# Kernel optimization log

Measured on AMD Instinct MI355X. Metric: run time of the kernel, lower is better.

The kernel has to match this reference:

```python
import jax, jax.numpy as jnp
import numpy as np

N_ITEMS = 7000
N_USERS = 30000
N_NODES = N_ITEMS + N_USERS  # 37000
D = 128        # embed_dim == user_embed_dim
E = 400000     # num edges
R = 10         # n_relation (num ratings)
NB = 8         # num_bases
B = 512        # batch of conversations
L = 100        # max context items per sample


def setup_inputs() -> dict:
    key = jax.random.key(0)
    ks = jax.random.split(key, 16)
    # edges: item (source) -> user (target), disjoint id ranges as in load_data
    src = jax.random.randint(ks[0], (E,), 0, N_ITEMS)
    dst = jax.random.randint(ks[1], (E,), N_ITEMS, N_NODES)
    edge_index = jnp.stack([src, dst]).astype(jnp.int64)
    edge_type = jax.random.randint(ks[2], (E,), 0, R).astype(jnp.int64)

    def make_ctx(k1, k2):
        c = jax.random.randint(k1, (B, L), 0, N_ITEMS)
        drop = jax.random.uniform(k2, (B, L)) < 0.3  # -1 padding as in batch lists
        return jnp.where(drop, -1, c).astype(jnp.int64)

    ctx_init = make_ctx(ks[3], ks[4])
    ctx_resp = make_ctx(ks[5], ks[6])

    s = 0.02
    basis = jax.random.normal(ks[7], (NB, N_NODES, D), jnp.float32) * s
    comp = jax.random.normal(ks[8], (R, NB), jnp.float32) * s
    root = jax.random.normal(ks[9], (N_NODES, D), jnp.float32) * s
    bias = jnp.zeros((D,), jnp.float32)
    attn_a = jax.random.normal(ks[10], (D, D), jnp.float32) * s
    attn_b = jax.random.normal(ks[11], (D,), jnp.float32) * s
    fc1_w = jax.random.normal(ks[12], (D, D), jnp.float32) * s
    fc1_b = jnp.zeros((D,), jnp.float32)
    fc2_w = jax.random.normal(ks[13], (D, D), jnp.float32) * s
    fc2_b = jnp.zeros((D,), jnp.float32)
    efc1_w = jax.random.normal(ks[14], (2 * D, D), jnp.float32) * s
    efc1_b = jnp.zeros((D,), jnp.float32)
    efc2_w = jax.random.normal(ks[15], (D, D), jnp.float32) * s
    efc2_b = jnp.zeros((D,), jnp.float32)
    return dict(edge_index=edge_index, edge_type=edge_type, ctx_init=ctx_init,
                ctx_resp=ctx_resp, basis=basis, comp=comp, root=root, bias=bias,
                attn_a=attn_a, attn_b=attn_b, fc1_w=fc1_w, fc1_b=fc1_b,
                fc2_w=fc2_w, fc2_b=fc2_b, efc1_w=efc1_w, efc1_b=efc1_b,
                efc2_w=efc2_w, efc2_b=efc2_b)


def _rgcn(basis, comp, root, bias, edge_index, edge_type):
    # RGCNConv with x=None: per-edge message W_{r_e}[src_e], mean-aggregated
    # per (target, relation), summed over relations, plus root lookup + bias.
    src, dst = edge_index[0], edge_index[1]
    nb, n, d = basis.shape
    r = comp.shape[0]
    cpe = comp[edge_type]  # [E, NB]
    msg = jnp.zeros((src.shape[0], d), basis.dtype)
    for b in range(nb):  # small fixed basis count; avoids [E,NB,D] gather
        msg = msg + cpe[:, b:b + 1] * basis[b][src]
    seg = dst * r + edge_type  # per-(node, relation) segment for mean aggr
    sums = jax.ops.segment_sum(msg, seg, num_segments=n * r).reshape(n, r, d)
    cnt = jax.ops.segment_sum(jnp.ones_like(edge_type, basis.dtype), seg,
                              num_segments=n * r).reshape(n, r, 1)
    return root + bias + (sums / jnp.maximum(cnt, 1.0)).sum(axis=1)  # [N, D]


def _item_user_means(node_emb, edge_index):
    # mean over users connected to each item (edge_idx[1][edge_idx[0]==item])
    src, dst = edge_index[0], edge_index[1]
    isum = jax.ops.segment_sum(node_emb[dst], src, num_segments=N_ITEMS)
    icnt = jax.ops.segment_sum(jnp.ones_like(src, node_emb.dtype), src,
                               num_segments=N_ITEMS)
    item_mean = isum / jnp.maximum(icnt, 1.0)[:, None]  # [N_ITEMS, D]
    return item_mean, icnt > 0


def _attn_pool(ctx, item_mean, item_has_users, attn_a, attn_b):
    # SelfAttentionBatch over each sample's item reps (padding/-1 & degree-0
    # items masked out; all-empty samples -> zeros, as in original).
    valid = ctx >= 0
    idx = jnp.clip(ctx, 0, N_ITEMS - 1)
    h = item_mean[idx]                       # [B, L, D]
    valid = valid & item_has_users[idx]
    e = jnp.einsum('bld,d->bl', jnp.tanh(jnp.einsum('bld,de->ble', h, attn_a)),
                   attn_b)
    attn = jax.nn.softmax(jnp.where(valid, e, -1e9), axis=-1)
    attn = jnp.where(valid, attn, 0.0)
    return jnp.einsum('bl,bld->bd', attn, h)  # [B, D]


def _project(x, w1, b1, w2, b2):
    # fc1 -> relu -> fc2 -> relu (as in _project_user_interaction_*)
    return jax.nn.relu(jax.nn.relu(x @ w1 + b1) @ w2 + b2)


def reference(edge_index, edge_type, ctx_init, ctx_resp, basis, comp, root,
              bias, attn_a, attn_b, fc1_w, fc1_b, fc2_w, fc2_b, efc1_w,
              efc1_b, efc2_w, efc2_b):
    node_emb = _rgcn(basis, comp, root, bias, edge_index, edge_type)
    item_mean, item_has = _item_user_means(node_emb, edge_index)
    p_init = _project(_attn_pool(ctx_init, item_mean, item_has, attn_a, attn_b),
                      fc1_w, fc1_b, fc2_w, fc2_b)
    p_resp = _project(_attn_pool(ctx_resp, item_mean, item_has, attn_a, attn_b),
                      fc1_w, fc1_b, fc2_w, fc2_b)
    both = jnp.concatenate([p_init, p_resp], axis=1)  # [B, 2D]
    profile = _project(both, efc1_w, efc1_b, efc2_w, efc2_b)  # [B, D]
    return profile, p_init, p_resp
```

## Files before the change

### kernel.cpp

```cpp
#include <hip/hip_runtime.h>
#include <math.h>

typedef unsigned int uint;

#define N_ITEMS 7000
#define N_NODES 37000
#define N_USERS 30000
#define DIM     128
#define HD      64
#define NREL    10
#define NBASES  8
#define BATCH   512
#define CTXL    100
#define E_MAX   400000

#define UCAP    64
#define ICAP    128

#define OFF_CNT    0
#define OFF_ICNT   (OFF_CNT + N_USERS * NREL)
#define OFF_UCNT   (OFF_ICNT + N_ITEMS)
#define ZERO_ELEMS (OFF_UCNT + N_USERS)
#define OFF_ICSR   ZERO_ELEMS
#define OFF_UCSR   (OFF_ICSR + N_ITEMS * ICAP)
#define OFF_WC     (OFF_UCSR + N_USERS * UCAP)
#define OFF_ACC    (OFF_WC + NREL * N_ITEMS * HD)
#define OFF_MEAN   (OFF_ACC + N_USERS * HD)
#define OFF_SCORE  (OFF_MEAN + N_ITEMS * HD)

__device__ __forceinline__ float2 bf2f(uint p) {
  float2 r;
  r.x = __uint_as_float(p << 16);
  r.y = __uint_as_float(p & 0xffff0000u);
  return r;
}
__device__ __forceinline__ uint f2bf(float x, float y) {
  uint a = __float_as_uint(x), b = __float_as_uint(y);
  a += 0x7fffu + ((a >> 16) & 1u);
  b += 0x7fffu + ((b >> 16) & 1u);
  return (a >> 16) | (b & 0xffff0000u);
}

__device__ __forceinline__ float wave_sum(float v) {
#pragma unroll
  for (int o = 1; o < 64; o <<= 1) v += __shfl_xor(v, o, 64);
  return v;
}
__device__ __forceinline__ float wave_max(float v) {
#pragma unroll
  for (int o = 1; o < 64; o <<= 1) v = fmaxf(v, __shfl_xor(v, o, 64));
  return v;
}

#define COMBINE_BLOCKS (N_ITEMS / 4)
__global__ __launch_bounds__(256) void k_initfill(const float* __restrict__ basis,
                                                  const float* __restrict__ comp,
                                                  uint* __restrict__ Wc,
                                                  const int* __restrict__ ei,
                                                  const int* __restrict__ et, int E,
                                                  int* __restrict__ cnt,
                                                  int* __restrict__ icnt,
                                                  int* __restrict__ ucnt,
                                                  int* __restrict__ icsr,
                                                  int* __restrict__ ucsr) {
  int tid = threadIdx.x;
  if (blockIdx.x < COMBINE_BLOCKS) {
    int i = blockIdx.x * 4 + (tid >> 6);
    int lane = tid & 63;
    float2 bb[NBASES];
#pragma unroll
    for (int b = 0; b < NBASES; ++b)
      bb[b] = ((const float2*)basis)[((size_t)b * N_NODES + i) * HD + lane];
#pragma unroll
    for (int r = 0; r < NREL; ++r) {
      float sx = 0.f, sy = 0.f;
#pragma unroll
      for (int b = 0; b < NBASES; ++b) {
        float c = comp[r * NBASES + b];
        sx = fmaf(c, bb[b].x, sx);
        sy = fmaf(c, bb[b].y, sy);
      }
      Wc[((size_t)i * NREL + r) * HD + lane] = f2bf(sx, sy);
    }
  } else {
    int e = (blockIdx.x - COMBINE_BLOCKS) * 256 + tid;
    if (e < E) {
      int s  = ei[e];
      int u0 = ei[E + e] - N_ITEMS;
      int t  = et[e];
      atomicAdd(&cnt[u0 * NREL + t], 1);
      int si = atomicAdd(&icnt[s], 1);
      if (si < ICAP) icsr[s * ICAP + si] = u0;
      int su = atomicAdd(&ucnt[u0], 1);
      if (su < UCAP) ucsr[u0 * UCAP + su] = s | (t << 16);
    }
  }
}

__global__ __launch_bounds__(256, 4) void k_useragg(const int* __restrict__ ucnt,
                                                    const int* __restrict__ ucsr,
                                                    const int* __restrict__ cnt,
                                                    const uint* __restrict__ Wc,
                                                    const float* __restrict__ root,
                                                    uint* __restrict__ acc) {
  int tid = threadIdx.x;
  int wid = tid >> 6, lane = tid & 63;
  int uA = blockIdx.x * 8 + wid * 2;
  int uB = uA + 1;
  int degA = ucnt[uA]; if (degA > UCAP) degA = UCAP;
  int degB = ucnt[uB]; if (degB > UCAP) degB = UCAP;
  float wlA = 0.f, wlB = 0.f;
  if (lane < NREL) {
    int cA = cnt[uA * NREL + lane];
    int cB = cnt[uB * NREL + lane];
    wlA = (cA > 0) ? 1.0f / (float)cA : 0.0f;
    wlB = (cB > 0) ? 1.0f / (float)cB : 0.0f;
  }
  int plA = ucsr[uA * UCAP + lane];
  int plB = ucsr[uB * UCAP + lane];

  float2 avA[4], avB[4];
#pragma unroll
  for (int k = 0; k < 4; ++k) {
    avA[k].x = 0.f; avA[k].y = 0.f;
    avB[k].x = 0.f; avB[k].y = 0.f;
  }
  int mmax = (degA > degB) ? degA : degB;
#pragma unroll 1
  for (int kk = 0; kk < mmax; kk += 16) {
    uint qA[16], qB[16];
#pragma unroll
    for (int k = 0; k < 16; ++k) {
      int idx = kk + k;
      int p = (idx < degA) ? __shfl(plA, idx & 63) : 0;
      qA[k] = Wc[((size_t)(p & 0xffff) * NREL + (p >> 16)) * HD + lane];
    }
#pragma unroll
    for (int k = 0; k < 16; ++k) {
      int idx = kk + k;
      int p = (idx < degB) ? __shfl(plB, idx & 63) : 0;
      qB[k] = Wc[((size_t)(p & 0xffff) * NREL + (p >> 16)) * HD + lane];
    }
#pragma unroll
    for (int k = 0; k < 16; ++k) {
      int idx = kk + k;
      int p = __shfl(plA, idx & 63);
      float w = (idx < degA) ? __shfl(wlA, p >> 16) : 0.f;
      float2 f = bf2f(qA[k]);
      avA[k & 3].x = fmaf(w, f.x, avA[k & 3].x);
      avA[k & 3].y = fmaf(w, f.y, avA[k & 3].y);
    }
#pragma unroll
    for (int k = 0; k < 16; ++k) {
      int idx = kk + k;
      int p = __shfl(plB, idx & 63);
      float w = (idx < degB) ? __shfl(wlB, p >> 16) : 0.f;
      float2 f = bf2f(qB[k]);
      avB[k & 3].x = fmaf(w, f.x, avB[k & 3].x);
      avB[k & 3].y = fmaf(w, f.y, avB[k & 3].y);
    }
  }
  float2 rtA = ((const float2*)root)[(size_t)(N_ITEMS + uA) * HD + lane];
  float2 rtB = ((const float2*)root)[(size_t)(N_ITEMS + uB) * HD + lane];
  rtA.x += (avA[0].x + avA[1].x) + (avA[2].x + avA[3].x);
  rtA.y += (avA[0].y + avA[1].y) + (avA[2].y + avA[3].y);
  rtB.x += (avB[0].x + avB[1].x) + (avB[2].x + avB[3].x);
  rtB.y += (avB[0].y + avB[1].y) + (avB[2].y + avB[3].y);
  acc[(size_t)uA * HD + lane] = f2bf(rtA.x, rtA.y);
  acc[(size_t)uB * HD + lane] = f2bf(rtB.x, rtB.y);
}

__global__ __launch_bounds__(256, 4) void k_itemagg(const int* __restrict__ icnt,
                                                    const int* __restrict__ icsr,
                                                    const uint* __restrict__ acc,
                                                    const float* __restrict__ bias,
                                                    const float* __restrict__ attn_a,
                                                    const float* __restrict__ attn_b,
                                                    uint* __restrict__ mean,
                                                    float* __restrict__ score) {
  int tid = threadIdx.x;
  int wid = tid >> 6, lane = tid & 63;
  int iA = blockIdx.x * 8 + wid * 2;
  int iB = iA + 1;
  int degA = icnt[iA], degB = icnt[iB];
  int dcA = (degA > ICAP) ? ICAP : degA;
  int dcB = (degB > ICAP) ? ICAP : degB;
  int plA0 = icsr[iA * ICAP + lane];
  int plA1 = icsr[iA * ICAP + 64 + lane];
  int plB0 = icsr[iB * ICAP + lane];
  int plB1 = icsr[iB * ICAP + 64 + lane];

  float2 avA[4], avB[4];
#pragma unroll
  for (int k = 0; k < 4; ++k) {
    avA[k].x = 0.f; avA[k].y = 0.f;
    avB[k].x = 0.f; avB[k].y = 0.f;
  }
  int mmax = (dcA > dcB) ? dcA : dcB;
#pragma unroll 1
  for (int kk = 0; kk < mmax; kk += 16) {
    int plAc = (kk < 64) ? plA0 : plA1;
    int plBc = (kk < 64) ? plB0 : plB1;
    uint qA[16], qB[16];
#pragma unroll
    for (int k = 0; k < 16; ++k) {
      int idx = kk + k;
      int u0 = (idx < dcA) ? __shfl(plAc, idx & 63) : 0;
      qA[k] = acc[(size_t)u0 * HD + lane];
    }
#pragma unroll
    for (int k = 0; k < 16; ++k) {
      int idx = kk + k;
      int u0 = (idx < dcB) ? __shfl(plBc, idx & 63) : 0;
      qB[k] = acc[(size_t)u0 * HD + lane];
    }
#pragma unroll
    for (int k = 0; k < 16; ++k) {
      int idx = kk + k;
      float w = (idx < dcA) ? 1.0f : 0.0f;
      float2 f = bf2f(qA[k]);
      avA[k & 3].x = fmaf(w, f.x, avA[k & 3].x);
      avA[k & 3].y = fmaf(w, f.y, avA[k & 3].y);
    }
#pragma unroll
    for (int k = 0; k < 16; ++k) {
      int idx = kk + k;
      float w = (idx < dcB) ? 1.0f : 0.0f;
      float2 f = bf2f(qB[k]);
      avB[k & 3].x = fmaf(w, f.x, avB[k & 3].x);
      avB[k & 3].y = fmaf(w, f.y, avB[k & 3].y);
    }
  }
  float sxA = (avA[0].x + avA[1].x) + (avA[2].x + avA[3].x);
  float syA = (avA[0].y + avA[1].y) + (avA[2].y + avA[3].y);
  float sxB = (avB[0].x + avB[1].x) + (avB[2].x + avB[3].x);
  float syB = (avB[0].y + avB[1].y) + (avB[2].y + avB[3].y);
  float2 bv = ((const float2*)bias)[lane];
  float2 mvA = {0.f, 0.f}, mvB = {0.f, 0.f};
  if (degA > 0) {
    float inv = 1.0f / (float)degA;
    mvA.x = sxA * inv + bv.x;
    mvA.y = syA * inv + bv.y;
  }
  if (degB > 0) {
    float inv = 1.0f / (float)degB;
    mvB.x = sxB * inv + bv.x;
    mvB.y = syB * inv + bv.y;
  }
  mean[(size_t)iA * HD + lane] = f2bf(mvA.x, mvA.y);
  mean[(size_t)iB * HD + lane] = f2bf(mvB.x, mvB.y);

  float z0A = 0.f, z1A = 0.f, z0B = 0.f, z1B = 0.f;
#pragma unroll 8
  for (int k2 = 0; k2 < HD; ++k2) {
    float2 w0 = ((const float2*)attn_a)[(size_t)(2 * k2) * HD + lane];
    float2 w1 = ((const float2*)attn_a)[(size_t)(2 * k2 + 1) * HD + lane];
    float hxA = __shfl(mvA.x, k2), hyA = __shfl(mvA.y, k2);
    float hxB = __shfl(mvB.x, k2), hyB = __shfl(mvB.y, k2);
    z0A = fmaf(hxA, w0.x, z0A); z1A = fmaf(hxA, w0.y, z1A);
    z0A = fmaf(hyA, w1.x, z0A); z1A = fmaf(hyA, w1.y, z1A);
    z0B = fmaf(hxB, w0.x, z0B); z1B = fmaf(hxB, w0.y, z1B);
    z0B = fmaf(hyB, w1.x, z0B); z1B = fmaf(hyB, w1.y, z1B);
  }
  float2 ab = ((const float2*)attn_b)[lane];
  float vA = wave_sum(tanhf(z0A) * ab.x + tanhf(z1A) * ab.y);
  float vB = wave_sum(tanhf(z0B) * ab.x + tanhf(z1B) * ab.y);
  if (lane == 0) {
    score[iA] = (degA > 0) ? vA : -1e9f;
    score[iB] = (degB > 0) ? vB : -1e9f;
  }
}

__global__ __launch_bounds__(128) void k_batch2(const int* __restrict__ ctx0,
                                                const int* __restrict__ ctx1,
                                                const uint* __restrict__ mean,
                                                const float* __restrict__ score,
                                                const float* __restrict__ fc1_w,
                                                const float* __restrict__ fc1_b,
                                                const float* __restrict__ fc2_w,
                                                const float* __restrict__ fc2_b,
                                                const float* __restrict__ efc1_w,
                                                const float* __restrict__ efc1_b,
                                                const float* __restrict__ efc2_w,
                                                const float* __restrict__ efc2_b,
                                                float* __restrict__ out) {
  __shared__ float2 shp[2][HD];
  int b = blockIdx.x;
  int wv = threadIdx.x >> 6;
  int lane = threadIdx.x & 63;
  float2* out2 = (float2*)out;

  const int* cx = (wv ? ctx1 : ctx0) + (size_t)b * CTXL;
  int id0 = cx[lane];
  float e0 = (id0 >= 0) ? score[id0] : -1e9f;
  int id1 = -1;
  float e1 = -3.0e38f;
  if (lane < CTXL - 64) {
    id1 = cx[64 + lane];
    e1 = (id1 >= 0) ? score[id1] : -1e9f;
  }
  float mx = wave_max(fmaxf(e0, e1));
  float x0 = expf(e0 - mx);
  float x1 = (lane < CTXL - 64) ? expf(e1 - mx) : 0.f;
  float inv = 1.0f / wave_sum(x0 + x1);
  float w0 = (id0 >= 0) ? x0 * inv : 0.f;
  float w1 = (id1 >= 0) ? x1 * inv : 0.f;
  int i0 = (id0 >= 0) ? id0 : 0;
  int i1 = (id1 >= 0) ? id1 : 0;

  float2 av[4];
#pragma unroll
  for (int k = 0; k < 4; ++k) { av[k].x = 0.f; av[k].y = 0.f; }
  for (int j = 0; j < 64; j += 4) {
#pragma unroll
    for (int k = 0; k < 4; ++k) {
      int ii = __shfl(i0, j + k);
      float ww = __shfl(w0, j + k);
      float2 f = bf2f(mean[(size_t)ii * HD + lane]);
      av[k].x = fmaf(ww, f.x, av[k].x);
      av[k].y = fmaf(ww, f.y, av[k].y);
    }
  }
  for (int j = 0; j < CTXL - 64; j += 4) {
#pragma unroll
    for (int k = 0; k < 4; ++k) {
      int ii = __shfl(i1, j + k);
      float ww = __shfl(w1, j + k);
      float2 f = bf2f(mean[(size_t)ii * HD + lane]);
      av[k].x = fmaf(ww, f.x, av[k].x);
      av[k].y = fmaf(ww, f.y, av[k].y);
    }
  }
  float2 pool;
  pool.x = (av[0].x + av[1].x) + (av[2].x + av[3].x);
  pool.y = (av[0].y + av[1].y) + (av[2].y + av[3].y);

  float2 z = ((const float2*)fc1_b)[lane];
#pragma unroll 8
  for (int k2 = 0; k2 < HD; ++k2) {
    float hx = __shfl(pool.x, k2);
    float hy = __shfl(pool.y, k2);
    float2 wa = ((const float2*)fc1_w)[(size_t)(2 * k2) * HD + lane];
    float2 wb = ((const float2*)fc1_w)[(size_t)(2 * k2 + 1) * HD + lane];
    z.x = fmaf(hx, wa.x, z.x); z.y = fmaf(hx, wa.y, z.y);
    z.x = fmaf(hy, wb.x, z.x); z.y = fmaf(hy, wb.y, z.y);
  }
  z.x = fmaxf(z.x, 0.f);
  z.y = fmaxf(z.y, 0.f);

  float2 z2 = ((const float2*)fc2_b)[lane];
#pragma unroll 8
  for (int k2 = 0; k2 < HD; ++k2) {
    float hx = __shfl(z.x, k2);
    float hy = __shfl(z.y, k2);
    float2 wa = ((const float2*)fc2_w)[(size_t)(2 * k2) * HD + lane];
    float2 wb = ((const float2*)fc2_w)[(size_t)(2 * k2 + 1) * HD + lane];
    z2.x = fmaf(hx, wa.x, z2.x); z2.y = fmaf(hx, wa.y, z2.y);
    z2.x = fmaf(hy, wb.x, z2.x); z2.y = fmaf(hy, wb.y, z2.y);
  }
  z2.x = fmaxf(z2.x, 0.f);
  z2.y = fmaxf(z2.y, 0.f);
  out2[((size_t)(1 + wv) * BATCH + b) * HD + lane] = z2;
  shp[wv][lane] = z2;
  __syncthreads();

  if (wv == 0) {
    float2 p0 = shp[0][lane];
    float2 p1 = shp[1][lane];
    float2 zz = ((const float2*)efc1_b)[lane];
#pragma unroll 8
    for (int k2 = 0; k2 < HD; ++k2) {
      float hx = __shfl(p0.x, k2);
      float hy = __shfl(p0.y, k2);
      float2 wa = ((const float2*)efc1_w)[(size_t)(2 * k2) * HD + lane];
      float2 wb = ((const float2*)efc1_w)[(size_t)(2 * k2 + 1) * HD + lane];
      zz.x = fmaf(hx, wa.x, zz.x); zz.y = fmaf(hx, wa.y, zz.y);
      zz.x = fmaf(hy, wb.x, zz.x); zz.y = fmaf(hy, wb.y, zz.y);
    }
#pragma unroll 8
    for (int k2 = 0; k2 < HD; ++k2) {
      float hx = __shfl(p1.x, k2);
      float hy = __shfl(p1.y, k2);
      float2 wa = ((const float2*)efc1_w)[(size_t)(DIM + 2 * k2) * HD + lane];
      float2 wb = ((const float2*)efc1_w)[(size_t)(DIM + 2 * k2 + 1) * HD + lane];
      zz.x = fmaf(hx, wa.x, zz.x); zz.y = fmaf(hx, wa.y, zz.y);
      zz.x = fmaf(hy, wb.x, zz.x); zz.y = fmaf(hy, wb.y, zz.y);
    }
    zz.x = fmaxf(zz.x, 0.f);
    zz.y = fmaxf(zz.y, 0.f);

    float2 zf = ((const float2*)efc2_b)[lane];
#pragma unroll 8
    for (int k2 = 0; k2 < HD; ++k2) {
      float hx = __shfl(zz.x, k2);
      float hy = __shfl(zz.y, k2);
      float2 wa = ((const float2*)efc2_w)[(size_t)(2 * k2) * HD + lane];
      float2 wb = ((const float2*)efc2_w)[(size_t)(2 * k2 + 1) * HD + lane];
      zf.x = fmaf(hx, wa.x, zf.x); zf.y = fmaf(hx, wa.y, zf.y);
      zf.x = fmaf(hy, wb.x, zf.x); zf.y = fmaf(hy, wb.y, zf.y);
    }
    zf.x = fmaxf(zf.x, 0.f);
    zf.y = fmaxf(zf.y, 0.f);
    out2[(size_t)b * HD + lane] = zf;
  }
}

extern "C" void kernel_launch(void* const* d_in, const int* in_sizes, int n_in,
                              void* d_out, int out_size, void* d_ws, size_t ws_size,
                              hipStream_t stream) {
  const int*   ei     = (const int*)d_in[0];
  const int*   et     = (const int*)d_in[1];
  const int*   ctx0   = (const int*)d_in[2];
  const int*   ctx1   = (const int*)d_in[3];
  const float* basis  = (const float*)d_in[4];
  const float* comp   = (const float*)d_in[5];
  const float* root   = (const float*)d_in[6];
  const float* bias   = (const float*)d_in[7];
  const float* attn_a = (const float*)d_in[8];
  const float* attn_b = (const float*)d_in[9];
  const float* fc1_w  = (const float*)d_in[10];
  const float* fc1_b  = (const float*)d_in[11];
  const float* fc2_w  = (const float*)d_in[12];
  const float* fc2_b  = (const float*)d_in[13];
  const float* efc1_w = (const float*)d_in[14];
  const float* efc1_b = (const float*)d_in[15];
  const float* efc2_w = (const float*)d_in[16];
  const float* efc2_b = (const float*)d_in[17];
  float* out = (float*)d_out;

  const int E = in_sizes[1];

  float* ws   = (float*)d_ws;
  int*  cnt   = (int*)(ws + OFF_CNT);
  int*  icnt  = (int*)(ws + OFF_ICNT);
  int*  ucnt  = (int*)(ws + OFF_UCNT);
  int*  icsr  = (int*)(ws + OFF_ICSR);
  int*  ucsr  = (int*)(ws + OFF_UCSR);
  uint* Wc    = (uint*)(ws + OFF_WC);
  uint* acc   = (uint*)(ws + OFF_ACC);
  uint* mean  = (uint*)(ws + OFF_MEAN);
  float* score = ws + OFF_SCORE;

  hipMemsetAsync(d_ws, 0, (size_t)ZERO_ELEMS * sizeof(float), stream);

  int countBlocks = (E + 255) / 256;
  k_initfill<<<COMBINE_BLOCKS + countBlocks, 256, 0, stream>>>(
      basis, comp, Wc, ei, et, E, cnt, icnt, ucnt, icsr, ucsr);
  k_useragg<<<N_USERS / 8, 256, 0, stream>>>(ucnt, ucsr, cnt, Wc, root, acc);
  k_itemagg<<<N_ITEMS / 8, 256, 0, stream>>>(icnt, icsr, acc, bias, attn_a,
                                             attn_b, mean, score);
  k_batch2<<<BATCH, 128, 0, stream>>>(ctx0, ctx1, mean, score, fc1_w, fc1_b,
                                      fc2_w, fc2_b, efc1_w, efc1_b, efc2_w,
                                      efc2_b, out);
}
```

Before: 387.4 us.

## Fuse all stages into one persistent cooperative kernel with grid syncs

Replaces the memset and four separate kernel launches with a single cooperative persistent kernel. Work is distributed with grid-stride loops, and stages are separated by grid.sync plus threadfence. The aim is to remove launch gaps and the separate memset. In exchange, the grid is capped at occupancy-limited block counts, which can reduce parallelism for the gather-heavy stages, and each grid barrier has its own cost.

Result: slower. 1.007 ms (+160.0%).

```diff
diff --git a/kernel.cpp b/kernel.cpp
--- a/kernel.cpp
+++ b/kernel.cpp
@@ -1,5 +1,8 @@
 #include <hip/hip_runtime.h>
+#include <hip/hip_cooperative_groups.h>
 #include <math.h>
+
+namespace cg = cooperative_groups;
 
 typedef unsigned int uint;
 
@@ -52,404 +55,415 @@
   return v;
 }
 
-#define COMBINE_BLOCKS (N_ITEMS / 4)
-__global__ __launch_bounds__(256) void k_initfill(const float* __restrict__ basis,
-                                                  const float* __restrict__ comp,
-                                                  uint* __restrict__ Wc,
-                                                  const int* __restrict__ ei,
-                                                  const int* __restrict__ et, int E,
-                                                  int* __restrict__ cnt,
-                                                  int* __restrict__ icnt,
-                                                  int* __restrict__ ucnt,
-                                                  int* __restrict__ icsr,
-                                                  int* __restrict__ ucsr) {
-  int tid = threadIdx.x;
-  if (blockIdx.x < COMBINE_BLOCKS) {
-    int i = blockIdx.x * 4 + (tid >> 6);
-    int lane = tid & 63;
+struct KParams {
+  const int*   ei;
+  const int*   et;
+  const int*   ctx0;
+  const int*   ctx1;
+  const float* basis;
+  const float* comp;
+  const float* root;
+  const float* bias;
+  const float* attn_a;
+  const float* attn_b;
+  const float* fc1_w;
+  const float* fc1_b;
+  const float* fc2_w;
+  const float* fc2_b;
+  const float* efc1_w;
+  const float* efc1_b;
+  const float* efc2_w;
+  const float* efc2_b;
+  float*       out;
+  float*       ws;
+  int          E;
+};
+
+__global__ __launch_bounds__(256, 4) void k_all(KParams p) {
+  int*  cnt   = (int*)(p.ws + OFF_CNT);
+  int*  icnt  = (int*)(p.ws + OFF_ICNT);
+  int*  ucnt  = (int*)(p.ws + OFF_UCNT);
+  int*  icsr  = (int*)(p.ws + OFF_ICSR);
+  int*  ucsr  = (int*)(p.ws + OFF_UCSR);
+  uint* Wc    = (uint*)(p.ws + OFF_WC);
+  uint* acc   = (uint*)(p.ws + OFF_ACC);
+  uint* mean  = (uint*)(p.ws + OFF_MEAN);
+  float* score = p.ws + OFF_SCORE;
+
+  const int tid  = threadIdx.x;
+  const int lane = tid & 63;
+  const int wid  = tid >> 6;
+  const int gsize = gridDim.x * 256;
+  const int gtid  = blockIdx.x * 256 + tid;
+  const int W  = gridDim.x * 4;
+  const int gw = blockIdx.x * 4 + wid;
+
+  __shared__ float2 shp[2][2][HD];
+
+  cg::grid_group grid = cg::this_grid();
+
+  {
+    int* wsz = (int*)p.ws;
+    for (int i = gtid; i < ZERO_ELEMS; i += gsize) wsz[i] = 0;
+  }
+  __threadfence();
+  grid.sync();
+
+  for (int i = gw; i < N_ITEMS; i += W) {
     float2 bb[NBASES];
 #pragma unroll
     for (int b = 0; b < NBASES; ++b)
-      bb[b] = ((const float2*)basis)[((size_t)b * N_NODES + i) * HD + lane];
+      bb[b] = ((const float2*)p.basis)[((size_t)b * N_NODES + i) * HD + lane];
 #pragma unroll
     for (int r = 0; r < NREL; ++r) {
       float sx = 0.f, sy = 0.f;
 #pragma unroll
       for (int b = 0; b < NBASES; ++b) {
-        float c = comp[r * NBASES + b];
+        float c = p.comp[r * NBASES + b];
         sx = fmaf(c, bb[b].x, sx);
         sy = fmaf(c, bb[b].y, sy);
       }
       Wc[((size_t)i * NREL + r) * HD + lane] = f2bf(sx, sy);
     }
-  } else {
-    int e = (blockIdx.x - COMBINE_BLOCKS) * 256 + tid;
-    if (e < E) {
-      int s  = ei[e];
-      int u0 = ei[E + e] - N_ITEMS;
-      int t  = et[e];
-      atomicAdd(&cnt[u0 * NREL + t], 1);
-      int si = atomicAdd(&icnt[s], 1);
-      if (si < ICAP) icsr[s * ICAP + si] = u0;
-      int su = atomicAdd(&ucnt[u0], 1);
-      if (su < UCAP) ucsr[u0 * UCAP + su] = s | (t << 16);
-    }
-  }
-}
-
-__global__ __launch_bounds__(256, 4) void k_useragg(const int* __restrict__ ucnt,
-                                                    const int* __restrict__ ucsr,
-                                                    const int* __restrict__ cnt,
-                                                    const uint* __restrict__ Wc,
-                                                    const float* __restrict__ root,
-                                                    uint* __restrict__ acc) {
-  int tid = threadIdx.x;
-  int wid = tid >> 6, lane = tid & 63;
-  int uA = blockIdx.x * 8 + wid * 2;
-  int uB = uA + 1;
-  int degA = ucnt[uA]; if (degA > UCAP) degA = UCAP;
-  int degB = ucnt[uB]; if (degB > UCAP) degB = UCAP;
-  float wlA = 0.f, wlB = 0.f;
-  if (lane < NREL) {
-    int cA = cnt[uA * NREL + lane];
-    int cB = cnt[uB * NREL + lane];
-    wlA = (cA > 0) ? 1.0f / (float)cA : 0.0f;
-    wlB = (cB > 0) ? 1.0f / (float)cB : 0.0f;
-  }
-  int plA = ucsr[uA * UCAP + lane];
-  int plB = ucsr[uB * UCAP + lane];
-
-  float2 avA[4], avB[4];
-#pragma unroll
-  for (int k = 0; k < 4; ++k) {
-    avA[k].x = 0.f; avA[k].y = 0.f;
-    avB[k].x = 0.f; avB[k].y = 0.f;
-  }
-  int mmax = (degA > degB) ? degA : degB;
+  }
+  for (int e = gtid; e < p.E; e += gsize) {
+    int s  = p.ei[e];
+    int u0 = p.ei[p.E + e] - N_ITEMS;
+    int t  = p.et[e];
+    atomicAdd(&cnt[u0 * NREL + t], 1);
+    int si = atomicAdd(&icnt[s], 1);
+    if (si < ICAP) icsr[s * ICAP + si] = u0;
+    int su = atomicAdd(&ucnt[u0], 1);
+    if (su < UCAP) ucsr[u0 * UCAP + su] = s | (t << 16);
+  }
+  __threadfence();
+  grid.sync();
+
+  for (int u = gw * 2; u < N_USERS; u += W * 2) {
+    int uA = u, uB = u + 1;
+    int degA = ucnt[uA]; if (degA > UCAP) degA = UCAP;
+    int degB = ucnt[uB]; if (degB > UCAP) degB = UCAP;
+    float wlA = 0.f, wlB = 0.f;
+    if (lane < NREL) {
+      int cA = cnt[uA * NREL + lane];
+      int cB = cnt[uB * NREL + lane];
+      wlA = (cA > 0) ? 1.0f / (float)cA : 0.0f;
+      wlB = (cB > 0) ? 1.0f / (float)cB : 0.0f;
+    }
+    int plA = ucsr[uA * UCAP + lane];
+    int plB = ucsr[uB * UCAP + lane];
+
+    float2 avA[4], avB[4];
+#pragma unroll
+    for (int k = 0; k < 4; ++k) {
+      avA[k].x = 0.f; avA[k].y = 0.f;
+      avB[k].x = 0.f; avB[k].y = 0.f;
+    }
+    int mmax = (degA > degB) ? degA : degB;
 #pragma unroll 1
-  for (int kk = 0; kk < mmax; kk += 16) {
-    uint qA[16], qB[16];
-#pragma unroll
-    for (int k = 0; k < 16; ++k) {
-      int idx = kk + k;
-      int p = (idx < degA) ? __shfl(plA, idx & 63) : 0;
-      qA[k] = Wc[((size_t)(p & 0xffff) * NREL + (p >> 16)) * HD + lane];
-    }
-#pragma unroll
-    for (int k = 0; k < 16; ++k) {
-      int idx = kk + k;
-      int p = (idx < degB) ? __shfl(plB, idx & 63) : 0;
-      qB[k] = Wc[((size_t)(p & 0xffff) * NREL + (p >> 16)) * HD + lane];
-    }
-#pragma unroll
-    for (int k = 0; k < 16; ++k) {
-      int idx = kk + k;
-      int p = __shfl(plA, idx & 63);
-      float w = (idx < degA) ? __shfl(wlA, p >> 16) : 0.f;
-      float2 f = bf2f(qA[k]);
-      avA[k & 3].x = fmaf(w, f.x, avA[k & 3].x);
-      avA[k & 3].y = fmaf(w, f.y, avA[k & 3].y);
-    }
-#pragma unroll
-    for (int k = 0; k < 16; ++k) {
-      int idx = kk + k;
-      int p = __shfl(plB, idx & 63);
-      float w = (idx < degB) ? __shfl(wlB, p >> 16) : 0.f;
-      float2 f = bf2f(qB[k]);
-      avB[k & 3].x = fmaf(w, f.x, avB[k & 3].x);
-      avB[k & 3].y = fmaf(w, f.y, avB[k & 3].y);
-    }
-  }
-  float2 rtA = ((const float2*)root)[(size_t)(N_ITEMS + uA) * HD + lane];
-  float2 rtB = ((const float2*)root)[(size_t)(N_ITEMS + uB) * HD + lane];
-  rtA.x += (avA[0].x + avA[1].x) + (avA[2].x + avA[3].x);
-  rtA.y += (avA[0].y + avA[1].y) + (avA[2].y + avA[3].y);
-  rtB.x += (avB[0].x + avB[1].x) + (avB[2].x + avB[3].x);
-  rtB.y += (avB[0].y + avB[1].y) + (avB[2].y + avB[3].y);
-  acc[(size_t)uA * HD + lane] = f2bf(rtA.x, rtA.y);
-  acc[(size_t)uB * HD + lane] = f2bf(rtB.x, rtB.y);
-}
-
-__global__ __launch_bounds__(256, 4) void k_itemagg(const int* __restrict__ icnt,
-                                                    const int* __restrict__ icsr,
-                                                    const uint* __restrict__ acc,
-                                                    const float* __restrict__ bias,
-                                                    const float* __restrict__ attn_a,
-                                                    const float* __restrict__ attn_b,
-                                                    uint* __restrict__ mean,
-                                                    float* __restrict__ score) {
-  int tid = threadIdx.x;
-  int wid = tid >> 6, lane = tid & 63;
-  int iA = blockIdx.x * 8 + wid * 2;
-  int iB = iA + 1;
-  int degA = icnt[iA], degB = icnt[iB];
-  int dcA = (degA > ICAP) ? ICAP : degA;
-  int dcB = (degB > ICAP) ? ICAP : degB;
-  int plA0 = icsr[iA * ICAP + lane];
-  int plA1 = icsr[iA * ICAP + 64 + lane];
-  int plB0 = icsr[iB * ICAP + lane];
-  int plB1 = icsr[iB * ICAP + 64 + lane];
-
-  float2 avA[4], avB[4];
-#pragma unroll
-  for (int k = 0; k < 4; ++k) {
-    avA[k].x = 0.f; avA[k].y = 0.f;
-    avB[k].x = 0.f; avB[k].y = 0.f;
-  }
-  int mmax = (dcA > dcB) ? dcA : dcB;
+    for (int kk = 0; kk < mmax; kk += 16) {
+      uint qA[16], qB[16];
+#pragma unroll
+      for (int k = 0; k < 16; ++k) {
+        int idx = kk + k;
+        int pp = (idx < degA) ? __shfl(plA, idx & 63) : 0;
+        qA[k] = Wc[((size_t)(pp & 0xffff) * NREL + (pp >> 16)) * HD + lane];
+      }
+#pragma unroll
+      for (int k = 0; k < 16; ++k) {
+        int idx = kk + k;
+        int pp = (idx < degB) ? __shfl(plB, idx & 63) : 0;
+        qB[k] = Wc[((size_t)(pp & 0xffff) * NREL + (pp >> 16)) * HD + lane];
+      }
+#pragma unroll
+      for (int k = 0; k < 16; ++k) {
+        int idx = kk + k;
+        int pp = __shfl(plA, idx & 63);
+        float w = (idx < degA) ? __shfl(wlA, pp >> 16) : 0.f;
+        float2 f = bf2f(qA[k]);
+        avA[k & 3].x = fmaf(w, f.x, avA[k & 3].x);
+        avA[k & 3].y = fmaf(w, f.y, avA[k & 3].y);
+      }
+#pragma unroll
+      for (int k = 0; k < 16; ++k) {
+        int idx = kk + k;
+        int pp = __shfl(plB, idx & 63);
+        float w = (idx < degB) ? __shfl(wlB, pp >> 16) : 0.f;
+        float2 f = bf2f(qB[k]);
+        avB[k & 3].x = fmaf(w, f.x, avB[k & 3].x);
+        avB[k & 3].y = fmaf(w, f.y, avB[k & 3].y);
+      }
+    }
+    float2 rtA = ((const float2*)p.root)[(size_t)(N_ITEMS + uA) * HD + lane];
+    float2 rtB = ((const float2*)p.root)[(size_t)(N_ITEMS + uB) * HD + lane];
+    rtA.x += (avA[0].x + avA[1].x) + (avA[2].x + avA[3].x);
+    rtA.y += (avA[0].y + avA[1].y) + (avA[2].y + avA[3].y);
+    rtB.x += (avB[0].x + avB[1].x) + (avB[2].x + avB[3].x);
+    rtB.y += (avB[0].y + avB[1].y) + (avB[2].y + avB[3].y);
+    acc[(size_t)uA * HD + lane] = f2bf(rtA.x, rtA.y);
+    acc[(size_t)uB * HD + lane] = f2bf(rtB.x, rtB.y);
+  }
+  __threadfence();
+  grid.sync();
+
+  for (int i = gw * 2; i < N_ITEMS; i += W * 2) {
+    int iA = i, iB = i + 1;
+    int degA = icnt[iA], degB = icnt[iB];
+    int dcA = (degA > ICAP) ? ICAP : degA;
+    int dcB = (degB > ICAP) ? ICAP : degB;
+    int plA0 = icsr[iA * ICAP + lane];
+    int plA1 = icsr[iA * ICAP + 64 + lane];
+    int plB0 = icsr[iB * ICAP + lane];
+    int plB1 = icsr[iB * ICAP + 64 + lane];
+
+    float2 avA[4], avB[4];
+#pragma unroll
+    for (int k = 0; k < 4; ++k) {
+      avA[k].x = 0.f; avA[k].y = 0.f;
+      avB[k].x = 0.f; avB[k].y = 0.f;
+    }
+    int mmax = (dcA > dcB) ? dcA : dcB;
 #pragma unroll 1
-  for (int kk = 0; kk < mmax; kk += 16) {
-    int plAc = (kk < 64) ? plA0 : plA1;
-    int plBc = (kk < 64) ? plB0 : plB1;
-    uint qA[16], qB[16];
-#pragma unroll
-    for (int k = 0; k < 16; ++k) {
-      int idx = kk + k;
-      int u0 = (idx < dcA) ? __shfl(plAc, idx & 63) : 0;
-      qA[k] = acc[(size_t)u0 * HD + lane];
-    }
-#pragma unroll
-    for (int k = 0; k < 16; ++k) {
-      int idx = kk + k;
-      int u0 = (idx < dcB) ? __shfl(plBc, idx & 63) : 0;
-      qB[k] = acc[(size_t)u0 * HD + lane];
-    }
-#pragma unroll
-    for (int k = 0; k < 16; ++k) {
-      int idx = kk + k;
-      float w = (idx < dcA) ? 1.0f : 0.0f;
-      float2 f = bf2f(qA[k]);
-      avA[k & 3].x = fmaf(w, f.x, avA[k & 3].x);
-      avA[k & 3].y = fmaf(w, f.y, avA[k & 3].y);
-    }
-#pragma unroll
-    for (int k = 0; k < 16; ++k) {
-      int idx = kk + k;
-      float w = (idx < dcB) ? 1.0f : 0.0f;
-      float2 f = bf2f(qB[k]);
-      avB[k & 3].x = fmaf(w, f.x, avB[k & 3].x);
-      avB[k & 3].y = fmaf(w, f.y, avB[k & 3].y);
-    }
-  }
-  float sxA = (avA[0].x + avA[1].x) + (avA[2].x + avA[3].x);
-  float syA = (avA[0].y + avA[1].y) + (avA[2].y + avA[3].y);
-  float sxB = (avB[0].x + avB[1].x) + (avB[2].x + avB[3].x);
-  float syB = (avB[0].y + avB[1].y) + (avB[2].y + avB[3].y);
-  float2 bv = ((const float2*)bias)[lane];
-  float2 mvA = {0.f, 0.f}, mvB = {0.f, 0.f};
-  if (degA > 0) {
-    float inv = 1.0f / (float)degA;
-    mvA.x = sxA * inv + bv.x;
-    mvA.y = syA * inv + bv.y;
-  }
-  if (degB > 0) {
-    float inv = 1.0f / (float)degB;
-    mvB.x = sxB * inv + bv.x;
-    mvB.y = syB * inv + bv.y;
-  }
-  mean[(size_t)iA * HD + lane] = f2bf(mvA.x, mvA.y);
-  mean[(size_t)iB * HD + lane] = f2bf(mvB.x, mvB.y);
-
-  float z0A = 0.f, z1A = 0.f, z0B = 0.f, z1B = 0.f;
-#pragma unroll 8
-  for (int k2 = 0; k2 < HD; ++k2) {
-    float2 w0 = ((const float2*)attn_a)[(size_t)(2 * k2) * HD + lane];
-    float2 w1 = ((const float2*)attn_a)[(size_t)(2 * k2 + 1) * HD + lane];
-    float hxA = __shfl(mvA.x, k2), hyA = __shfl(mvA.y, k2);
-    float hxB = __shfl(mvB.x, k2), hyB = __shfl(mvB.y, k2);
-    z0A = fmaf(hxA, w0.x, z0A); z1A = fmaf(hxA, w0.y, z1A);
-    z0A = fmaf(hyA, w1.x, z0A); z1A = fmaf(hyA, w1.y, z1A);
-    z0B = fmaf(hxB, w0.x, z0B); z1B = fmaf(hxB, w0.y, z1B);
-    z0B = fmaf(hyB, w1.x, z0B); z1B = fmaf(hyB, w1.y, z1B);
-  }
-  float2 ab = ((const float2*)attn_b)[lane];
-  float vA = wave_sum(tanhf(z0A) * ab.x + tanhf(z1A) * ab.y);
-  float vB = wave_sum(tanhf(z0B) * ab.x + tanhf(z1B) * ab.y);
-  if (lane == 0) {
-    score[iA] = (degA > 0) ? vA : -1e9f;
-    score[iB] = (degB > 0) ? vB : -1e9f;
-  }
-}
-
-__global__ __launch_bounds__(128) void k_batch2(const int* __restrict__ ctx0,
-                                                const int* __restrict__ ctx1,
-                                                const uint* __restrict__ mean,
-                                                const float* __restrict__ score,
-                                                const float* __restrict__ fc1_w,
-                                                const float* __restrict__ fc1_b,
-                                                const float* __restrict__ fc2_w,
-                                                const float* __restrict__ fc2_b,
-                                                const float* __restrict__ efc1_w,
-                                                const float* __restrict__ efc1_b,
-                                                const float* __restrict__ efc2_w,
-                                                const float* __restrict__ efc2_b,
-                                                float* __restrict__ out) {
-  __shared__ float2 shp[2][HD];
-  int b = blockIdx.x;
-  int wv = threadIdx.x >> 6;
-  int lane = threadIdx.x & 63;
-  float2* out2 = (float2*)out;
-
-  const int* cx = (wv ? ctx1 : ctx0) + (size_t)b * CTXL;
-  int id0 = cx[lane];
-  float e0 = (id0 >= 0) ? score[id0] : -1e9f;
-  int id1 = -1;
-  float e1 = -3.0e38f;
-  if (lane < CTXL - 64) {
-    id1 = cx[64 + lane];
-    e1 = (id1 >= 0) ? score[id1] : -1e9f;
-  }
-  float mx = wave_max(fmaxf(e0, e1));
-  float x0 = expf(e0 - mx);
-  float x1 = (lane < CTXL - 64) ? expf(e1 - mx) : 0.f;
-  float inv = 1.0f / wave_sum(x0 + x1);
-  float w0 = (id0 >= 0) ? x0 * inv : 0.f;
-  float w1 = (id1 >= 0) ? x1 * inv : 0.f;
-  int i0 = (id0 >= 0) ? id0 : 0;
-  int i1 = (id1 >= 0) ? id1 : 0;
-
-  float2 av[4];
-#pragma unroll
-  for (int k = 0; k < 4; ++k) { av[k].x = 0.f; av[k].y = 0.f; }
-  for (int j = 0; j < 64; j += 4) {
-#pragma unroll
-    for (int k = 0; k < 4; ++k) {
-      int ii = __shfl(i0, j + k);
-      float ww = __shfl(w0, j + k);
-      float2 f = bf2f(mean[(size_t)ii * HD + lane]);
-      av[k].x = fmaf(ww, f.x, av[k].x);
-      av[k].y = fmaf(ww, f.y, av[k].y);
-    }
-  }
-  for (int j = 0; j < CTXL - 64; j += 4) {
-#pragma unroll
-    for (int k = 0; k < 4; ++k) {
-      int ii = __shfl(i1, j + k);
-      float ww = __shfl(w1, j + k);
-      float2 f = bf2f(mean[(size_t)ii * HD + lane]);
-      av[k].x = fmaf(ww, f.x, av[k].x);
-      av[k].y = fmaf(ww, f.y, av[k].y);
-    }
-  }
-  float2 pool;
-  pool.x = (av[0].x + av[1].x) + (av[2].x + av[3].x);
-  pool.y = (av[0].y + av[1].y) + (av[2].y + av[3].y);
-
-  float2 z = ((const float2*)fc1_b)[lane];
-#pragma unroll 8
-  for (int k2 = 0; k2 < HD; ++k2) {
-    float hx = __shfl(pool.x, k2);
-    float hy = __shfl(pool.y, k2);
-    float2 wa = ((const float2*)fc1_w)[(size_t)(2 * k2) * HD + lane];
-    float2 wb = ((const float2*)fc1_w)[(size_t)(2 * k2 + 1) * HD + lane];
-    z.x = fmaf(hx, wa.x, z.x); z.y = fmaf(hx, wa.y, z.y);
-    z.x = fmaf(hy, wb.x, z.x); z.y = fmaf(hy, wb.y, z.y);
-  }
-  z.x = fmaxf(z.x, 0.f);
-  z.y = fmaxf(z.y, 0.f);
-
-  float2 z2 = ((const float2*)fc2_b)[lane];
-#pragma unroll 8
-  for (int k2 = 0; k2 < HD; ++k2) {
-    float hx = __shfl(z.x, k2);
-    float hy = __shfl(z.y, k2);
-    float2 wa = ((const float2*)fc2_w)[(size_t)(2 * k2) * HD + lane];
-    float2 wb = ((const float2*)fc2_w)[(size_t)(2 * k2 + 1) * HD + lane];
-    z2.x = fmaf(hx, wa.x, z2.x); z2.y = fmaf(hx, wa.y, z2.y);
-    z2.x = fmaf(hy, wb.x, z2.x); z2.y = fmaf(hy, wb.y, z2.y);
-  }
-  z2.x = fmaxf(z2.x, 0.f);
-  z2.y = fmaxf(z2.y, 0.f);
-  out2[((size_t)(1 + wv) * BATCH + b) * HD + lane] = z2;
-  shp[wv][lane] = z2;
-  __syncthreads();
-
-  if (wv == 0) {
-    float2 p0 = shp[0][lane];
-    float2 p1 = shp[1][lane];
-    float2 zz = ((const float2*)efc1_b)[lane];
+    for (int kk = 0; kk < mmax; kk += 16) {
+      int plAc = (kk < 64) ? plA0 : plA1;
+      int plBc = (kk < 64) ? plB0 : plB1;
+      uint qA[16], qB[16];
+#pragma unroll
+      for (int k = 0; k < 16; ++k) {
+        int idx = kk + k;
+        int u0 = (idx < dcA) ? __shfl(plAc, idx & 63) : 0;
+        qA[k] = acc[(size_t)u0 * HD + lane];
+      }
+#pragma unroll
+      for (int k = 0; k < 16; ++k) {
+        int idx = kk + k;
+        int u0 = (idx < dcB) ? __shfl(plBc, idx & 63) : 0;
+        qB[k] = acc[(size_t)u0 * HD + lane];
+      }
+#pragma unroll
+      for (int k = 0; k < 16; ++k) {
+        int idx = kk + k;
+        float w = (idx < dcA) ? 1.0f : 0.0f;
+        float2 f = bf2f(qA[k]);
+        avA[k & 3].x = fmaf(w, f.x, avA[k & 3].x);
+        avA[k & 3].y = fmaf(w, f.y, avA[k & 3].y);
+      }
+#pragma unroll
+      for (int k = 0; k < 16; ++k) {
+        int idx = kk + k;
+        float w = (idx < dcB) ? 1.0f : 0.0f;
+        float2 f = bf2f(qB[k]);
+        avB[k & 3].x = fmaf(w, f.x, avB[k & 3].x);
+        avB[k & 3].y = fmaf(w, f.y, avB[k & 3].y);
+      }
+    }
+    float sxA = (avA[0].x + avA[1].x) + (avA[2].x + avA[3].x);
+    float syA = (avA[0].y + avA[1].y) + (avA[2].y + avA[3].y);
+    float sxB = (avB[0].x + avB[1].x) + (avB[2].x + avB[3].x);
+    float syB = (avB[0].y + avB[1].y) + (avB[2].y + avB[3].y);
+    float2 bv = ((const float2*)p.bias)[lane];
+    float2 mvA = {0.f, 0.f}, mvB = {0.f, 0.f};
+    if (degA > 0) {
+      float inv = 1.0f / (float)degA;
+      mvA.x = sxA * inv + bv.x;
+      mvA.y = syA * inv + bv.y;
+    }
+    if (degB > 0) {
+      float inv = 1.0f / (float)degB;
+      mvB.x = sxB * inv + bv.x;
+      mvB.y = syB * inv + bv.y;
+    }
+    mean[(size_t)iA * HD + lane] = f2bf(mvA.x, mvA.y);
+    mean[(size_t)iB * HD + lane] = f2bf(mvB.x, mvB.y);
+
+    float z0A = 0.f, z1A = 0.f, z0B = 0.f, z1B = 0.f;
 #pragma unroll 8
     for (int k2 = 0; k2 < HD; ++k2) {
-      float hx = __shfl(p0.x, k2);
-      float hy = __shfl(p0.y, k2);
-      float2 wa = ((const float2*)efc1_w)[(size_t)(2 * k2) * HD + lane];
-      float2 wb = ((const float2*)efc1_w)[(size_t)(2 * k2 + 1) * HD + lane];
-      zz.x = fmaf(hx, wa.x, zz.x); zz.y = fmaf(hx, wa.y, zz.y);
-      zz.x = fmaf(hy, wb.x, zz.x); zz.y = fmaf(hy, wb.y, zz.y);
-    }
+      float2 w0 = ((const float2*)p.attn_a)[(size_t)(2 * k2) * HD + lane];
+      float2 w1 = ((const float2*)p.attn_a)[(size_t)(2 * k2 + 1) * HD + lane];
+      float hxA = __shfl(mvA.x, k2), hyA = __shfl(mvA.y, k2);
+      float hxB = __shfl(mvB.x, k2), hyB = __shfl(mvB.y, k2);
+      z0A = fmaf(hxA, w0.x, z0A); z1A = fmaf(hxA, w0.y, z1A);
+      z0A = fmaf(hyA, w1.x, z0A); z1A = fmaf(hyA, w1.y, z1A);
+      z0B = fmaf(hxB, w0.x, z0B); z1B = fmaf(hxB, w0.y, z1B);
+      z0B = fmaf(hyB, w1.x, z0B); z1B = fmaf(hyB, w1.y, z1B);
+    }
+    float2 ab = ((const float2*)p.attn_b)[lane];
+    float vA = wave_sum(tanhf(z0A) * ab.x + tanhf(z1A) * ab.y);
+    float vB = wave_sum(tanhf(z0B) * ab.x + tanhf(z1B) * ab.y);
+    if (lane == 0) {
+      score[iA] = (degA > 0) ? vA : -1e9f;
+      score[iB] = (degB > 0) ? vB : -1e9f;
+    }
+  }
+  __threadfence();
+  grid.sync();
+
+  float2* out2 = (float2*)p.out;
+  const int pairIdx = wid >> 1;
+  const int side    = wid & 1;
+  for (int bb = blockIdx.x; bb < BATCH / 2; bb += gridDim.x) {
+    int b = bb * 2 + pairIdx;
+
+    const int* cx = (side ? p.ctx1 : p.ctx0) + (size_t)b * CTXL;
+    int id0 = cx[lane];
+    float e0 = (id0 >= 0) ? score[id0] : -1e9f;
+    int id1 = -1;
+    float e1 = -3.0e38f;
+    if (lane < CTXL - 64) {
+      id1 = cx[64 + lane];
+      e1 = (id1 >= 0) ? score[id1] : -1e9f;
+    }
+    float mx = wave_max(fmaxf(e0, e1));
+    float x0 = expf(e0 - mx);
+    float x1 = (lane < CTXL - 64) ? expf(e1 - mx) : 0.f;
+    float inv = 1.0f / wave_sum(x0 + x1);
+    float w0 = (id0 >= 0) ? x0 * inv : 0.f;
+    float w1 = (id1 >= 0) ? x1 * inv : 0.f;
+    int i0 = (id0 >= 0) ? id0 : 0;
+    int i1 = (id1 >= 0) ? id1 : 0;
+
+    float2 av[4];
+#pragma unroll
+    for (int k = 0; k < 4; ++k) { av[k].x = 0.f; av[k].y = 0.f; }
+    for (int j = 0; j < 64; j += 4) {
+#pragma unroll
+      for (int k = 0; k < 4; ++k) {
+        int ii = __shfl(i0, j + k);
+        float ww = __shfl(w0, j + k);
+        float2 f = bf2f(mean[(size_t)ii * HD + lane]);
+        av[k].x = fmaf(ww, f.x, av[k].x);
+        av[k].y = fmaf(ww, f.y, av[k].y);
+      }
+    }
+    for (int j = 0; j < CTXL - 64; j += 4) {
+#pragma unroll
+      for (int k = 0; k < 4; ++k) {
+        int ii = __shfl(i1, j + k);
+        float ww = __shfl(w1, j + k);
+        float2 f = bf2f(mean[(size_t)ii * HD + lane]);
+        av[k].x = fmaf(ww, f.x, av[k].x);
+        av[k].y = fmaf(ww, f.y, av[k].y);
+      }
+    }
+    float2 pool;
+    pool.x = (av[0].x + av[1].x) + (av[2].x + av[3].x);
+    pool.y = (av[0].y + av[1].y) + (av[2].y + av[3].y);
+
+    float2 z = ((const float2*)p.fc1_b)[lane];
 #pragma unroll 8
     for (int k2 = 0; k2 < HD; ++k2) {
-      float hx = __shfl(p1.x, k2);
-      float hy = __shfl(p1.y, k2);
-      float2 wa = ((const float2*)efc1_w)[(size_t)(DIM + 2 * k2) * HD + lane];
-      float2 wb = ((const float2*)efc1_w)[(size_t)(DIM + 2 * k2 + 1) * HD + lane];
-      zz.x = fmaf(hx, wa.x, zz.x); zz.y = fmaf(hx, wa.y, zz.y);
-      zz.x = fmaf(hy, wb.x, zz.x); zz.y = fmaf(hy, wb.y, zz.y);
-    }
-    zz.x = fmaxf(zz.x, 0.f);
-    zz.y = fmaxf(zz.y, 0.f);
-
-    float2 zf = ((const float2*)efc2_b)[lane];
+      float hx = __shfl(pool.x, k2);
+      float hy = __shfl(pool.y, k2);
+      float2 wa = ((const float2*)p.fc1_w)[(size_t)(2 * k2) * HD + lane];
+      float2 wb = ((const float2*)p.fc1_w)[(size_t)(2 * k2 + 1) * HD + lane];
+      z.x = fmaf(hx, wa.x, z.x); z.y = fmaf(hx, wa.y, z.y);
+      z.x = fmaf(hy, wb.x, z.x); z.y = fmaf(hy, wb.y, z.y);
+    }
+    z.x = fmaxf(z.x, 0.f);
+    z.y = fmaxf(z.y, 0.f);
+
+    float2 z2 = ((const float2*)p.fc2_b)[lane];
 #pragma unroll 8
     for (int k2 = 0; k2 < HD; ++k2) {
-      float hx = __shfl(zz.x, k2);
-      float hy = __shfl(zz.y, k2);
-      float2 wa = ((const float2*)efc2_w)[(size_t)(2 * k2) * HD + lane];
-      float2 wb = ((const float2*)efc2_w)[(size_t)(2 * k2 + 1) * HD + lane];
-      zf.x = fmaf(hx, wa.x, zf.x); zf.y = fmaf(hx, wa.y, zf.y);
-      zf.x = fmaf(hy, wb.x, zf.x); zf.y = fmaf(hy, wb.y, zf.y);
-    }
-    zf.x = fmaxf(zf.x, 0.f);
-    zf.y = fmaxf(zf.y, 0.f);
-    out2[(size_t)b * HD + lane] = zf;
+      float hx = __shfl(z.x, k2);
+      float hy = __shfl(z.y, k2);
+      float2 wa = ((const float2*)p.fc2_w)[(size_t)(2 * k2) * HD + lane];
+      float2 wb = ((const float2*)p.fc2_w)[(size_t)(2 * k2 + 1) * HD + lane];
+      z2.x = fmaf(hx, wa.x, z2.x); z2.y = fmaf(hx, wa.y, z2.y);
+      z2.x = fmaf(hy, wb.x, z2.x); z2.y = fmaf(hy, wb.y, z2.y);
+    }
+    z2.x = fmaxf(z2.x, 0.f);
+    z2.y = fmaxf(z2.y, 0.f);
+    out2[((size_t)(1 + side) * BATCH + b) * HD + lane] = z2;
+    shp[pairIdx][side][lane] = z2;
+    __syncthreads();
+
+    if (side == 0) {
+      float2 p0 = shp[pairIdx][0][lane];
+      float2 p1 = shp[pairIdx][1][lane];
+      float2 zz = ((const float2*)p.efc1_b)[lane];
+#pragma unroll 8
+      for (int k2 = 0; k2 < HD; ++k2) {
+        float hx = __shfl(p0.x, k2);
+        float hy = __shfl(p0.y, k2);
+        float2 wa = ((const float2*)p.efc1_w)[(size_t)(2 * k2) * HD + lane];
+        float2 wb = ((const float2*)p.efc1_w)[(size_t)(2 * k2 + 1) * HD + lane];
+        zz.x = fmaf(hx, wa.x, zz.x); zz.y = fmaf(hx, wa.y, zz.y);
+        zz.x = fmaf(hy, wb.x, zz.x); zz.y = fmaf(hy, wb.y, zz.y);
+      }
+#pragma unroll 8
+      for (int k2 = 0; k2 < HD; ++k2) {
+        float hx = __shfl(p1.x, k2);
+        float hy = __shfl(p1.y, k2);
+        float2 wa = ((const float2*)p.efc1_w)[(size_t)(DIM + 2 * k2) * HD + lane];
+        float2 wb = ((const float2*)p.efc1_w)[(size_t)(DIM + 2 * k2 + 1) * HD + lane];
+        zz.x = fmaf(hx, wa.x, zz.x); zz.y = fmaf(hx, wa.y, zz.y);
+        zz.x = fmaf(hy, wb.x, zz.x); zz.y = fmaf(hy, wb.y, zz.y);
+      }
+      zz.x = fmaxf(zz.x, 0.f);
+      zz.y = fmaxf(zz.y, 0.f);
+
+      float2 zf = ((const float2*)p.efc2_b)[lane];
+#pragma unroll 8
+      for (int k2 = 0; k2 < HD; ++k2) {
+        float hx = __shfl(zz.x, k2);
+        float hy = __shfl(zz.y, k2);
+        float2 wa = ((const float2*)p.efc2_w)[(size_t)(2 * k2) * HD + lane];
+        float2 wb = ((const float2*)p.efc2_w)[(size_t)(2 * k2 + 1) * HD + lane];
+        zf.x = fmaf(hx, wa.x, zf.x); zf.y = fmaf(hx, wa.y, zf.y);
+        zf.x = fmaf(hy, wb.x, zf.x); zf.y = fmaf(hy, wb.y, zf.y);
+      }
+      zf.x = fmaxf(zf.x, 0.f);
+      zf.y = fmaxf(zf.y, 0.f);
+      out2[(size_t)b * HD + lane] = zf;
+    }
+    __syncthreads();
   }
 }
 
 extern "C" void kernel_launch(void* const* d_in, const int* in_sizes, int n_in,
                               void* d_out, int out_size, void* d_ws, size_t ws_size,
                               hipStream_t stream) {
-  const int*   ei     = (const int*)d_in[0];
-  const int*   et     = (const int*)d_in[1];
-  const int*   ctx0   = (const int*)d_in[2];
-  const int*   ctx1   = (const int*)d_in[3];
-  const float* basis  = (const float*)d_in[4];
-  const float* comp   = (const float*)d_in[5];
-  const float* root   = (const float*)d_in[6];
-  const float* bias   = (const float*)d_in[7];
-  const float* attn_a = (const float*)d_in[8];
-  const float* attn_b = (const float*)d_in[9];
-  const float* fc1_w  = (const float*)d_in[10];
-  const float* fc1_b  = (const float*)d_in[11];
-  const float* fc2_w  = (const float*)d_in[12];
-  const float* fc2_b  = (const float*)d_in[13];
-  const float* efc1_w = (const float*)d_in[14];
-  const float* efc1_b = (const float*)d_in[15];
-  const float* efc2_w = (const float*)d_in[16];
-  const float* efc2_b = (const float*)d_in[17];
-  float* out = (float*)d_out;
-
-  const int E = in_sizes[1];
-
-  float* ws   = (float*)d_ws;
-  int*  cnt   = (int*)(ws + OFF_CNT);
-  int*  icnt  = (int*)(ws + OFF_ICNT);
-  int*  ucnt  = (int*)(ws + OFF_UCNT);
-  int*  icsr  = (int*)(ws + OFF_ICSR);
-  int*  ucsr  = (int*)(ws + OFF_UCSR);
-  uint* Wc    = (uint*)(ws + OFF_WC);
-  uint* acc   = (uint*)(ws + OFF_ACC);
-  uint* mean  = (uint*)(ws + OFF_MEAN);
-  float* score = ws + OFF_SCORE;
-
-  hipMemsetAsync(d_ws, 0, (size_t)ZERO_ELEMS * sizeof(float), stream);
-
-  int countBlocks = (E + 255) / 256;
-  k_initfill<<<COMBINE_BLOCKS + countBlocks, 256, 0, stream>>>(
-      basis, comp, Wc, ei, et, E, cnt, icnt, ucnt, icsr, ucsr);
-  k_useragg<<<N_USERS / 8, 256, 0, stream>>>(ucnt, ucsr, cnt, Wc, root, acc);
-  k_itemagg<<<N_ITEMS / 8, 256, 0, stream>>>(icnt, icsr, acc, bias, attn_a,
-                                             attn_b, mean, score);
-  k_batch2<<<BATCH, 128, 0, stream>>>(ctx0, ctx1, mean, score, fc1_w, fc1_b,
-                                      fc2_w, fc2_b, efc1_w, efc1_b, efc2_w,
-                                      efc2_b, out);
-}
+  KParams prm;
+  prm.ei     = (const int*)d_in[0];
+  prm.et     = (const int*)d_in[1];
+  prm.ctx0   = (const int*)d_in[2];
+  prm.ctx1   = (const int*)d_in[3];
+  prm.basis  = (const float*)d_in[4];
+  prm.comp   = (const float*)d_in[5];
+  prm.root   = (const float*)d_in[6];
+  prm.bias   = (const float*)d_in[7];
+  prm.attn_a = (const float*)d_in[8];
+  prm.attn_b = (const float*)d_in[9];
+  prm.fc1_w  = (const float*)d_in[10];
+  prm.fc1_b  = (const float*)d_in[11];
+  prm.fc2_w  = (const float*)d_in[12];
+  prm.fc2_b  = (const float*)d_in[13];
+  prm.efc1_w = (const float*)d_in[14];
+  prm.efc1_b = (const float*)d_in[15];
+  prm.efc2_w = (const float*)d_in[16];
+  prm.efc2_b = (const float*)d_in[17];
+  prm.out    = (float*)d_out;
+  prm.ws     = (float*)d_ws;
+  prm.E      = in_sizes[1];
+
+  static int g_nblk = 0;
+  if (g_nblk == 0) {
+    int maxb = 0;
+    hipOccupancyMaxActiveBlocksPerMultiprocessor(&maxb, k_all, 256, 0);
+    if (maxb < 1) maxb = 1;
+    int dev = 0;
+    hipGetDevice(&dev);
+    hipDeviceProp_t prop;
+    hipGetDeviceProperties(&prop, dev);
+    int nb = prop.multiProcessorCount * maxb;
+    if (nb > 1024) nb = 1024;
+    if (nb < 64)  nb = 64;
+    g_nblk = nb;
+  }
+
+  void* kargs[] = { (void*)&prm };
+  hipLaunchCooperativeKernel((const void*)k_all, dim3(g_nblk), dim3(256), kargs,
+                             0, stream);
+}
```
